# Kernel optimization log

Measured on AMD Instinct MI355X. Metric: run time of the kernel, lower is better.

## Reference

```python
import jax, jax.numpy as jnp
import numpy as np

NUM_EXPERTS = 8
PHM_DIM = 4


def setup_inputs() -> dict:
    key = jax.random.key(0)
    k1, k2, k3, k4 = jax.random.split(key, 4)
    bsz, seq, D, O, E, p = 4, 2048, 2048, 2048, NUM_EXPERTS, PHM_DIM
    hidden_states = jax.random.normal(k1, (bsz, seq, D), dtype=jnp.float32)
    gate_w = jax.random.normal(k2, (D, E), dtype=jnp.float32) * 0.02
    phm_rule = jax.random.normal(k3, (E, p, p, p), dtype=jnp.float32) * 0.1
    W = jax.random.normal(k4, (E, p, D // p, O // p), dtype=jnp.float32) * 0.02
    b = jnp.zeros((E, O), dtype=jnp.float32)
    return {"hidden_states": hidden_states, "gate_w": gate_w,
            "phm_rule": phm_rule, "W": W, "b": b}


def reference(hidden_states, gate_w, phm_rule, W, b):
    bsz, seq, dim = hidden_states.shape
    E = gate_w.shape[1]
    x = hidden_states.reshape(-1, dim)                      # [T, D]
    logits = x @ gate_w                                     # [T, E]
    prob = jax.nn.softmax(logits, axis=-1)                  # [T, E]
    gate = jnp.argmax(prob, axis=-1)                        # [T]
    # load-balancing loss
    num_tokens = jnp.sum(jax.nn.one_hot(gate, E, dtype=jnp.int32), axis=0)  # [E]
    f = num_tokens.astype(prob.dtype)
    f = f / jnp.sum(f)
    P = jnp.mean(prob, axis=0)
    balance_loss = E * jnp.sum(P * f)
    # PHM weight per expert: H_e = sum_p kron(phm_rule[e,p], W[e,p]) -> [E, D, O]
    Wfull = jnp.einsum('epab,epij->eaibj', phm_rule, W).reshape(E, dim, -1)
    # dense evaluation of every expert on every token, then top-1 select
    all_out = jnp.einsum('td,edo->teo', x, Wfull) + b[None, :, :]  # [T, E, O]
    tok_prob = jnp.take_along_axis(prob, gate[:, None], axis=1)    # [T, 1]
    out = jnp.take_along_axis(all_out, gate[:, None, None], axis=1)[:, 0, :] * tok_prob
    out = out.reshape(bsz, seq, -1)
    return out, balance_loss, num_tokens
```

## Files before the change

### kernel.cpp

```cpp
#include <hip/hip_runtime.h>
#include <cstdint>
#include <cstddef>

typedef _Float16 f16;
typedef f16 f16x2 __attribute__((ext_vector_type(2)));
typedef f16 f16x4 __attribute__((ext_vector_type(4)));
typedef f16 f16x8 __attribute__((ext_vector_type(8)));
typedef float f32x4 __attribute__((ext_vector_type(4)));

#define NEXP 8
#define BM 128
#define BN 256
#define BK 32

__device__ __forceinline__ void async_cp16(void* lds, const void* gsrc) {
  __builtin_amdgcn_global_load_lds(
      (const __attribute__((address_space(1))) void*)gsrc,
      (__attribute__((address_space(3))) void*)lds, 16, 0, 0);
}

__global__ __launch_bounds__(256) void k_gate(
    const float* __restrict__ x, const float* __restrict__ gw,
    f16* __restrict__ xb, int* __restrict__ gate, float* __restrict__ scale,
    int* __restrict__ cnt, float* __restrict__ probsum, int D)
{
  __shared__ float ps[NEXP];
  __shared__ int pc[NEXP];
  int tid = threadIdx.x, lane = tid & 63, w = tid >> 6;
  if (tid < NEXP) { ps[tid] = 0.f; pc[tid] = 0; }
  __syncthreads();

  int t = blockIdx.x * 4 + w;
  const float* xr = x + (size_t)t * D;
  f16* xbr = xb + (size_t)t * D;

  float acc[NEXP] = {};
  for (int d0 = lane * 4; d0 < D; d0 += 256) {
    float4 v = *(const float4*)(xr + d0);
    f16x4 h; h[0] = (f16)v.x; h[1] = (f16)v.y; h[2] = (f16)v.z; h[3] = (f16)v.w;
    *(f16x4*)(xbr + d0) = h;
    const float* g0 = gw + (size_t)d0 * NEXP;
    float xv[4] = {v.x, v.y, v.z, v.w};
#pragma unroll
    for (int j = 0; j < 4; j++) {
      float4 ga = *(const float4*)(g0 + j * NEXP);
      float4 gb = *(const float4*)(g0 + j * NEXP + 4);
      acc[0] += xv[j] * ga.x; acc[1] += xv[j] * ga.y;
      acc[2] += xv[j] * ga.z; acc[3] += xv[j] * ga.w;
      acc[4] += xv[j] * gb.x; acc[5] += xv[j] * gb.y;
      acc[6] += xv[j] * gb.z; acc[7] += xv[j] * gb.w;
    }
  }
#pragma unroll
  for (int e = 0; e < NEXP; e++) {
    float v = acc[e];
    for (int o = 32; o > 0; o >>= 1) v += __shfl_xor(v, o);
    acc[e] = v;
  }
  if (lane == 0) {
    float m = acc[0]; int g = 0;
#pragma unroll
    for (int e = 1; e < NEXP; e++) if (acc[e] > m) { m = acc[e]; g = e; }
    float pr[NEXP]; float ssum = 0.f;
#pragma unroll
    for (int e = 0; e < NEXP; e++) { pr[e] = __expf(acc[e] - m); ssum += pr[e]; }
    float inv = 1.0f / ssum;
#pragma unroll
    for (int e = 0; e < NEXP; e++) atomicAdd(&ps[e], pr[e] * inv);
    atomicAdd(&pc[g], 1);
    gate[t] = g;
    scale[t] = pr[g] * inv;
  }
  __syncthreads();
  if (tid < NEXP) {
    atomicAdd(&probsum[tid], ps[tid]);
    atomicAdd(&cnt[tid], pc[tid]);
  }
}

__global__ __launch_bounds__(256) void k_wfull(
    const float* __restrict__ Wp, const float* __restrict__ rule,
    f16* __restrict__ wt, int Dp, int Op, int D, int O)
{
  int bid = blockIdx.x;
  int it = Dp >> 5, jt = Op >> 5;
  int itile = bid % it; bid /= it;
  int jtile = bid % jt; bid /= jt;
  int e = bid;
  int i0 = itile * 32, j0 = jtile * 32;

  __shared__ float Wt[4][32][33];
  int tid = threadIdx.x;
  for (int idx = tid; idx < 4096; idx += 256) {
    int p = idx >> 10, rem = idx & 1023, ii = rem >> 5, jj = rem & 31;
    Wt[p][ii][jj] = Wp[(size_t)((e * 4 + p) * Dp + i0 + ii) * Op + j0 + jj];
  }
  __syncthreads();

  int ii = (tid & 15) * 2, jjb = tid >> 4;
#pragma unroll
  for (int b = 0; b < 4; b++) {
    float s[4][4];
#pragma unroll
    for (int p = 0; p < 4; p++)
#pragma unroll
      for (int a = 0; a < 4; a++)
        s[p][a] = rule[((e * 4 + p) * 4 + a) * 4 + b];
#pragma unroll
    for (int a = 0; a < 4; a++) {
#pragma unroll
      for (int jp = 0; jp < 2; jp++) {
        int jj = jjb + jp * 16;
        float v0 = 0.f, v1 = 0.f;
#pragma unroll
        for (int p = 0; p < 4; p++) {
          v0 += s[p][a] * Wt[p][ii][jj];
          v1 += s[p][a] * Wt[p][ii + 1][jj];
        }
        size_t n = (size_t)b * Op + j0 + jj;
        size_t dd = (size_t)a * Dp + i0 + ii;
        f16x2 hv; hv[0] = (f16)v0; hv[1] = (f16)v1;
        *(f16x2*)(wt + ((size_t)e * O + n) * D + dd) = hv;
      }
    }
  }
}

__global__ void k_plan(const int* __restrict__ cnt, const float* __restrict__ probsum,
                       int* __restrict__ offs, int* __restrict__ ndesc,
                       int2* __restrict__ desc, float* __restrict__ otail, int T)
{
  if (threadIdx.x != 0 || blockIdx.x != 0) return;
  int off = 0, nd = 0; float loss = 0.f;
  for (int e = 0; e < NEXP; e++) {
    offs[e] = off;
    int c = cnt[e];
    loss += probsum[e] * (float)c;
    for (int m0 = 0; m0 < c; m0 += BM) { desc[nd] = make_int2(e, m0); nd++; }
    off += c;
  }
  offs[NEXP] = off;
  *ndesc = nd;
  float invT = 1.0f / (float)T;
  otail[0] = (float)NEXP * loss * invT * invT;
  for (int e = 0; e < NEXP; e++) otail[1 + e] = (float)cnt[e];
}

__global__ __launch_bounds__(256) void k_scatter(
    const int* __restrict__ gate, const int* __restrict__ offs,
    int* __restrict__ cursor, int* __restrict__ perm)
{
  int t = blockIdx.x * 256 + threadIdx.x;
  int g = gate[t];
  int lane = threadIdx.x & 63;
  int pos = 0;
#pragma unroll
  for (int e = 0; e < NEXP; e++) {
    unsigned long long mask = __ballot(g == e);
    if (mask == 0ull) continue;
    int leader = __ffsll((unsigned long long)mask) - 1;
    int base = 0;
    if (lane == leader) base = atomicAdd(&cursor[e], (int)__popcll(mask));
    base = __shfl(base, leader);
    if (g == e) {
      int below = (int)__popcll(mask & ((1ull << lane) - 1ull));
      pos = offs[e] + base + below;
    }
  }
  perm[pos] = t;
}

__global__ __launch_bounds__(256) void k_gemm(
    const f16* __restrict__ xb, const f16* __restrict__ wt,
    const float* __restrict__ bias, const int* __restrict__ perm,
    const int* __restrict__ cnt, const int* __restrict__ offs,
    const int* __restrict__ ndesc, const int2* __restrict__ desc,
    const float* __restrict__ scale, float* __restrict__ out, int D, int O)
{
  if ((int)blockIdx.y >= *ndesc) return;
  int2 dsc = desc[blockIdx.y];
  int e = dsc.x, m0 = dsc.y;
  int ce = cnt[e];
  int seg = offs[e];
  int n0 = blockIdx.x * BN;

  __shared__ f16 Al[2][BM * BK];
  __shared__ f16 Bl[2][BN * BK];
  __shared__ int tokS[BM];
  __shared__ float scS[BM];

  int tid = threadIdx.x;
  if (tid < BM) {
    int idx = m0 + tid; if (idx > ce - 1) idx = ce - 1;
    int tok = perm[seg + idx];
    tokS[tid] = tok;
    scS[tid] = scale[tok];
  }
  __syncthreads();

  int r = tid >> 2;
  int c = tid & 3;
  int gc = c ^ ((r >> 1) & 3);
  const f16* a1 = xb + (size_t)tokS[r] * D + gc * 8;
  const f16* a2 = xb + (size_t)tokS[r + 64] * D + gc * 8;
  const f16* bp0 = wt + ((size_t)e * O + n0 + r) * D + gc * 8;
  const f16* bp1 = wt + ((size_t)e * O + n0 + r + 64) * D + gc * 8;
  const f16* bp2 = wt + ((size_t)e * O + n0 + r + 128) * D + gc * 8;
  const f16* bp3 = wt + ((size_t)e * O + n0 + r + 192) * D + gc * 8;

  int lane = tid & 63;
  int w = tid >> 6;
  int wm = (w & 1) * 64, wn = (w >> 1) * 128;
  int lr = lane & 15, q = lane >> 4;
  int qs = q ^ ((lr >> 1) & 3);

  f32x4 acc[4][8] = {};
  int nk = D / BK;

#define STAGE(kk, p)                                              \
  do {                                                            \
    async_cp16(&Al[(p)][tid * 8], a1 + (kk) * BK);                \
    async_cp16(&Al[(p)][2048 + tid * 8], a2 + (kk) * BK);         \
    async_cp16(&Bl[(p)][tid * 8], bp0 + (kk) * BK);               \
    async_cp16(&Bl[(p)][2048 + tid * 8], bp1 + (kk) * BK);        \
    async_cp16(&Bl[(p)][4096 + tid * 8], bp2 + (kk) * BK);        \
    async_cp16(&Bl[(p)][6144 + tid * 8], bp3 + (kk) * BK);        \
  } while (0)

  STAGE(0, 0);
  STAGE(1, 1);

  for (int kk = 0; kk < nk; ++kk) {
    int p = kk & 1;
    if (kk + 1 < nk)
      asm volatile("s_waitcnt vmcnt(6)\n\ts_barrier" ::: "memory");
    else
      asm volatile("s_waitcnt vmcnt(0)\n\ts_barrier" ::: "memory");

    f16x8 af[4], bf[8];
#pragma unroll
    for (int mi = 0; mi < 4; mi++)
      af[mi] = *(const f16x8*)&Al[p][(wm + mi * 16 + lr) * BK + qs * 8];
#pragma unroll
    for (int ni = 0; ni < 8; ni++)
      bf[ni] = *(const f16x8*)&Bl[p][(wn + ni * 16 + lr) * BK + qs * 8];

    asm volatile("s_waitcnt lgkmcnt(0)\n\ts_barrier" ::: "memory");
    if (kk + 2 < nk) STAGE(kk + 2, p);

#pragma unroll
    for (int mi = 0; mi < 4; mi++)
#pragma unroll
      for (int ni = 0; ni < 8; ni++)
        acc[mi][ni] = __builtin_amdgcn_mfma_f32_16x16x32_f16(
            af[mi], bf[ni], acc[mi][ni], 0, 0, 0);
  }
#undef STAGE

  float bv[8];
#pragma unroll
  for (int ni = 0; ni < 8; ni++)
    bv[ni] = bias[(size_t)e * O + n0 + wn + ni * 16 + lr];
#pragma unroll
  for (int mi = 0; mi < 4; mi++) {
#pragma unroll
    for (int rg = 0; rg < 4; rg++) {
      int rl = wm + mi * 16 + q * 4 + rg;
      if (m0 + rl < ce) {
        float s = scS[rl];
        float* orow = out + (size_t)tokS[rl] * O + n0 + wn;
#pragma unroll
        for (int ni = 0; ni < 8; ni++)
          orow[ni * 16 + lr] = (acc[mi][ni][rg] + bv[ni]) * s;
      }
    }
  }
}

extern "C" void kernel_launch(void* const* d_in, const int* in_sizes, int n_in,
                              void* d_out, int out_size, void* d_ws, size_t ws_size,
                              hipStream_t stream)
{
  const float* x    = (const float*)d_in[0];
  const float* gw   = (const float*)d_in[1];
  const float* rule = (const float*)d_in[2];
  const float* W    = (const float*)d_in[3];
  const float* bias = (const float*)d_in[4];
  float* out = (float*)d_out;

  int D = in_sizes[1] / NEXP;
  int O = in_sizes[4] / NEXP;
  int T = in_sizes[0] / D;
  int Dp = D / 4, Op = O / 4;

  uint8_t* ws = (uint8_t*)d_ws;
  size_t off = 0;
  f16* xb = (f16*)(ws + off);  off += (size_t)T * D * 2;
  f16* wt = (f16*)(ws + off);  off += (size_t)NEXP * O * D * 2;
  int*   gate  = (int*)(ws + off);   off += (size_t)T * 4;
  float* scale = (float*)(ws + off); off += (size_t)T * 4;
  int*   perm  = (int*)(ws + off);   off += (size_t)T * 4;
  off = (off + 255) & ~(size_t)255;
  uint8_t* C = ws + off;
  int*   cnt     = (int*)(C + 0);
  float* probsum = (float*)(C + 32);
  int*   cursor  = (int*)(C + 64);
  int*   ndesc   = (int*)(C + 96);
  int*   offs    = (int*)(C + 128);
  int2*  desc    = (int2*)(C + 192);

  hipMemsetAsync(C, 0, 128, stream);

  k_gate<<<T / 4, 256, 0, stream>>>(x, gw, xb, gate, scale, cnt, probsum, D);
  k_wfull<<<NEXP * (Op / 32) * (Dp / 32), 256, 0, stream>>>(W, rule, wt, Dp, Op, D, O);
  k_plan<<<1, 1, 0, stream>>>(cnt, probsum, offs, ndesc, desc, out + (size_t)T * O, T);
  k_scatter<<<T / 256, 256, 0, stream>>>(gate, offs, cursor, perm);

  int maxdesc = T / BM + NEXP;
  k_gemm<<<dim3(O / BN, maxdesc), 256, 0, stream>>>(
      xb, wt, bias, perm, cnt, offs, ndesc, desc, scale, out, D, O);
}
```

Measured before the change: 389.1 us.

## Shrink GEMM N-tile, add triple-buffered pipeline, transpose gate weights, parallelize plan

The grouped expert GEMM now uses a 128x128 tile instead of 128x256 and a three-stage async LDS pipeline instead of double buffering. This aims for more blocks and more latency hiding, at the cost of lower per-block reuse of the A tile. The gate weights are transposed into workspace by a new small kernel so the gating dot products read them with coalesced float4 loads. The planning kernel now runs with 128 threads, building the plan in shared memory and writing the outputs in parallel.

```diff
diff --git a/kernel.cpp b/kernel.cpp
--- a/kernel.cpp
+++ b/kernel.cpp
@@ -10,8 +10,9 @@
 
 #define NEXP 8
 #define BM 128
-#define BN 256
+#define BN 128
 #define BK 32
+#define NSTAGE 3
 
 __device__ __forceinline__ void async_cp16(void* lds, const void* gsrc) {
   __builtin_amdgcn_global_load_lds(
@@ -19,8 +20,15 @@
       (__attribute__((address_space(3))) void*)lds, 16, 0, 0);
 }
 
+__global__ __launch_bounds__(256) void k_gwT(const float* __restrict__ gw,
+                                             float* __restrict__ gwT, int D) {
+  int i = blockIdx.x * 256 + threadIdx.x;
+  int e = i / D, d = i - e * D;
+  gwT[i] = gw[d * NEXP + e];
+}
+
 __global__ __launch_bounds__(256) void k_gate(
-    const float* __restrict__ x, const float* __restrict__ gw,
+    const float* __restrict__ x, const float* __restrict__ gwT,
     f16* __restrict__ xb, int* __restrict__ gate, float* __restrict__ scale,
     int* __restrict__ cnt, float* __restrict__ probsum, int D)
 {
@@ -39,16 +47,10 @@
     float4 v = *(const float4*)(xr + d0);
     f16x4 h; h[0] = (f16)v.x; h[1] = (f16)v.y; h[2] = (f16)v.z; h[3] = (f16)v.w;
     *(f16x4*)(xbr + d0) = h;
-    const float* g0 = gw + (size_t)d0 * NEXP;
-    float xv[4] = {v.x, v.y, v.z, v.w};
-#pragma unroll
-    for (int j = 0; j < 4; j++) {
-      float4 ga = *(const float4*)(g0 + j * NEXP);
-      float4 gb = *(const float4*)(g0 + j * NEXP + 4);
-      acc[0] += xv[j] * ga.x; acc[1] += xv[j] * ga.y;
-      acc[2] += xv[j] * ga.z; acc[3] += xv[j] * ga.w;
-      acc[4] += xv[j] * gb.x; acc[5] += xv[j] * gb.y;
-      acc[6] += xv[j] * gb.z; acc[7] += xv[j] * gb.w;
+#pragma unroll
+    for (int e = 0; e < NEXP; e++) {
+      float4 g = *(const float4*)(gwT + (size_t)e * D + d0);
+      acc[e] += v.x * g.x + v.y * g.y + v.z * g.z + v.w * g.w;
     }
   }
 #pragma unroll
@@ -126,24 +128,38 @@
   }
 }
 
-__global__ void k_plan(const int* __restrict__ cnt, const float* __restrict__ probsum,
-                       int* __restrict__ offs, int* __restrict__ ndesc,
-                       int2* __restrict__ desc, float* __restrict__ otail, int T)
-{
-  if (threadIdx.x != 0 || blockIdx.x != 0) return;
-  int off = 0, nd = 0; float loss = 0.f;
-  for (int e = 0; e < NEXP; e++) {
-    offs[e] = off;
-    int c = cnt[e];
-    loss += probsum[e] * (float)c;
-    for (int m0 = 0; m0 < c; m0 += BM) { desc[nd] = make_int2(e, m0); nd++; }
-    off += c;
-  }
-  offs[NEXP] = off;
-  *ndesc = nd;
-  float invT = 1.0f / (float)T;
-  otail[0] = (float)NEXP * loss * invT * invT;
-  for (int e = 0; e < NEXP; e++) otail[1 + e] = (float)cnt[e];
+__global__ __launch_bounds__(128) void k_plan(
+    const int* __restrict__ cnt, const float* __restrict__ probsum,
+    int* __restrict__ offs, int* __restrict__ ndesc,
+    int2* __restrict__ desc, float* __restrict__ otail, int T)
+{
+  __shared__ int soffs[NEXP + 1];
+  __shared__ int snd;
+  __shared__ float sloss;
+  __shared__ int2 sdesc[96];
+  int tid = threadIdx.x;
+  if (tid == 0) {
+    int off = 0, nd = 0; float loss = 0.f;
+    for (int e = 0; e < NEXP; e++) {
+      soffs[e] = off;
+      int c = cnt[e];
+      loss += probsum[e] * (float)c;
+      for (int m0 = 0; m0 < c; m0 += BM) { sdesc[nd] = make_int2(e, m0); nd++; }
+      off += c;
+    }
+    soffs[NEXP] = off;
+    snd = nd;
+    sloss = loss;
+  }
+  __syncthreads();
+  if (tid <= NEXP) offs[tid] = soffs[tid];
+  if (tid == 9) *ndesc = snd;
+  if (tid == 10) {
+    float invT = 1.0f / (float)T;
+    otail[0] = (float)NEXP * sloss * invT * invT;
+  }
+  if (tid >= 16 && tid < 16 + NEXP) otail[1 + tid - 16] = (float)cnt[tid - 16];
+  for (int i = tid; i < snd; i += 128) desc[i] = sdesc[i];
 }
 
 __global__ __launch_bounds__(256) void k_scatter(
@@ -184,8 +200,8 @@
   int seg = offs[e];
   int n0 = blockIdx.x * BN;
 
-  __shared__ f16 Al[2][BM * BK];
-  __shared__ f16 Bl[2][BN * BK];
+  __shared__ f16 Al[NSTAGE][BM * BK];
+  __shared__ f16 Bl[NSTAGE][BN * BK];
   __shared__ int tokS[BM];
   __shared__ float scS[BM];
 
@@ -203,63 +219,65 @@
   int gc = c ^ ((r >> 1) & 3);
   const f16* a1 = xb + (size_t)tokS[r] * D + gc * 8;
   const f16* a2 = xb + (size_t)tokS[r + 64] * D + gc * 8;
-  const f16* bp0 = wt + ((size_t)e * O + n0 + r) * D + gc * 8;
-  const f16* bp1 = wt + ((size_t)e * O + n0 + r + 64) * D + gc * 8;
-  const f16* bp2 = wt + ((size_t)e * O + n0 + r + 128) * D + gc * 8;
-  const f16* bp3 = wt + ((size_t)e * O + n0 + r + 192) * D + gc * 8;
+  const f16* b1 = wt + ((size_t)e * O + n0 + r) * D + gc * 8;
+  const f16* b2 = wt + ((size_t)e * O + n0 + r + 64) * D + gc * 8;
 
   int lane = tid & 63;
   int w = tid >> 6;
-  int wm = (w & 1) * 64, wn = (w >> 1) * 128;
+  int wm = (w & 1) * 64, wn = (w >> 1) * 64;
   int lr = lane & 15, q = lane >> 4;
   int qs = q ^ ((lr >> 1) & 3);
 
-  f32x4 acc[4][8] = {};
+  f32x4 acc[4][4] = {};
   int nk = D / BK;
 
-#define STAGE(kk, p)                                              \
-  do {                                                            \
-    async_cp16(&Al[(p)][tid * 8], a1 + (kk) * BK);                \
-    async_cp16(&Al[(p)][2048 + tid * 8], a2 + (kk) * BK);         \
-    async_cp16(&Bl[(p)][tid * 8], bp0 + (kk) * BK);               \
-    async_cp16(&Bl[(p)][2048 + tid * 8], bp1 + (kk) * BK);        \
-    async_cp16(&Bl[(p)][4096 + tid * 8], bp2 + (kk) * BK);        \
-    async_cp16(&Bl[(p)][6144 + tid * 8], bp3 + (kk) * BK);        \
+#define STAGE(kk, p)                                             \
+  do {                                                           \
+    async_cp16(&Al[(p)][tid * 8], a1 + (kk) * BK);               \
+    async_cp16(&Al[(p)][2048 + tid * 8], a2 + (kk) * BK);        \
+    async_cp16(&Bl[(p)][tid * 8], b1 + (kk) * BK);               \
+    async_cp16(&Bl[(p)][2048 + tid * 8], b2 + (kk) * BK);        \
   } while (0)
 
   STAGE(0, 0);
   STAGE(1, 1);
-
+  STAGE(2, 2);
+
+  int p = 0;
   for (int kk = 0; kk < nk; ++kk) {
-    int p = kk & 1;
-    if (kk + 1 < nk)
-      asm volatile("s_waitcnt vmcnt(6)\n\ts_barrier" ::: "memory");
+    int rem = nk - 1 - kk;
+    if (rem >= 2)
+      asm volatile("s_waitcnt vmcnt(8)\n\ts_barrier" ::: "memory");
+    else if (rem == 1)
+      asm volatile("s_waitcnt vmcnt(4)\n\ts_barrier" ::: "memory");
     else
       asm volatile("s_waitcnt vmcnt(0)\n\ts_barrier" ::: "memory");
 
-    f16x8 af[4], bf[8];
+    f16x8 af[4], bf[4];
 #pragma unroll
     for (int mi = 0; mi < 4; mi++)
       af[mi] = *(const f16x8*)&Al[p][(wm + mi * 16 + lr) * BK + qs * 8];
 #pragma unroll
-    for (int ni = 0; ni < 8; ni++)
+    for (int ni = 0; ni < 4; ni++)
       bf[ni] = *(const f16x8*)&Bl[p][(wn + ni * 16 + lr) * BK + qs * 8];
 
     asm volatile("s_waitcnt lgkmcnt(0)\n\ts_barrier" ::: "memory");
-    if (kk + 2 < nk) STAGE(kk + 2, p);
+    if (kk + NSTAGE < nk) STAGE(kk + NSTAGE, p);
 
 #pragma unroll
     for (int mi = 0; mi < 4; mi++)
 #pragma unroll
-      for (int ni = 0; ni < 8; ni++)
+      for (int ni = 0; ni < 4; ni++)
         acc[mi][ni] = __builtin_amdgcn_mfma_f32_16x16x32_f16(
             af[mi], bf[ni], acc[mi][ni], 0, 0, 0);
+
+    p++; if (p == NSTAGE) p = 0;
   }
 #undef STAGE
 
-  float bv[8];
-#pragma unroll
-  for (int ni = 0; ni < 8; ni++)
+  float bv[4];
+#pragma unroll
+  for (int ni = 0; ni < 4; ni++)
     bv[ni] = bias[(size_t)e * O + n0 + wn + ni * 16 + lr];
 #pragma unroll
   for (int mi = 0; mi < 4; mi++) {
@@ -270,7 +288,7 @@
         float s = scS[rl];
         float* orow = out + (size_t)tokS[rl] * O + n0 + wn;
 #pragma unroll
-        for (int ni = 0; ni < 8; ni++)
+        for (int ni = 0; ni < 4; ni++)
           orow[ni * 16 + lr] = (acc[mi][ni][rg] + bv[ni]) * s;
       }
     }
@@ -308,12 +326,14 @@
   int*   ndesc   = (int*)(C + 96);
   int*   offs    = (int*)(C + 128);
   int2*  desc    = (int2*)(C + 192);
+  float* gwT     = (float*)(C + 4096);
 
   hipMemsetAsync(C, 0, 128, stream);
 
-  k_gate<<<T / 4, 256, 0, stream>>>(x, gw, xb, gate, scale, cnt, probsum, D);
+  k_gwT<<<(NEXP * D) / 256, 256, 0, stream>>>(gw, gwT, D);
+  k_gate<<<T / 4, 256, 0, stream>>>(x, gwT, xb, gate, scale, cnt, probsum, D);
   k_wfull<<<NEXP * (Op / 32) * (Dp / 32), 256, 0, stream>>>(W, rule, wt, Dp, Op, D, O);
-  k_plan<<<1, 1, 0, stream>>>(cnt, probsum, offs, ndesc, desc, out + (size_t)T * O, T);
+  k_plan<<<1, 128, 0, stream>>>(cnt, probsum, offs, ndesc, desc, out + (size_t)T * O, T);
   k_scatter<<<T / 256, 256, 0, stream>>>(gate, offs, cursor, perm);
 
   int maxdesc = T / BM + NEXP;
```

Result: faster. 339.9 us (-12.6%).
